# Optimization experiments

Measured on AMD Instinct MI355X. Metric: run time of the kernel, lower is better.

The kernel has to match this reference:

```python
import jax, jax.numpy as jnp
import numpy as np
from jax import lax

A = 9                 # 3 ratios x 3 scales
STRIDE = 16
PRE_NMS = 6000
POST_NMS = 300
NMS_THRESH = 0.7
POOL = 7
SAMPLES = 2           # roi-align sampling ratio
N_CLASSES = 21


def _generate_anchors(base=16.0, ratios=(0.5, 1.0, 2.0), scales=(8.0, 16.0, 32.0)):
    ratios = np.asarray(ratios, np.float64)
    scales = np.asarray(scales, np.float64)
    ctr = (base - 1.0) / 2.0
    size = base * base
    ws = np.round(np.sqrt(size / ratios))
    hs = np.round(ws * ratios)
    out = []
    for w0, h0 in zip(ws, hs):
        w2 = w0 * scales
        h2 = h0 * scales
        out.append(np.stack([ctr - (w2 - 1) / 2, ctr - (h2 - 1) / 2,
                             ctr + (w2 - 1) / 2, ctr + (h2 - 1) / 2], 1))
    return np.concatenate(out, 0).astype(np.float32)  # [A,4]


def _decode(anchors, deltas):
    # bbox_transform_inv with +1 width/height convention
    w = anchors[:, 2] - anchors[:, 0] + 1.0
    h = anchors[:, 3] - anchors[:, 1] + 1.0
    cx = anchors[:, 0] + 0.5 * w
    cy = anchors[:, 1] + 0.5 * h
    pcx = deltas[:, 0] * w + cx
    pcy = deltas[:, 1] * h + cy
    pw = jnp.exp(deltas[:, 2]) * w
    ph = jnp.exp(deltas[:, 3]) * h
    return jnp.stack([pcx - 0.5 * pw, pcy - 0.5 * ph,
                      pcx + 0.5 * pw, pcy + 0.5 * ph], 1)


def _nms_keep(boxes, thresh):
    # greedy NMS over score-sorted boxes; precomputed [N,N] IoU (memory-bound)
    N = boxes.shape[0]
    x1, y1, x2, y2 = boxes[:, 0], boxes[:, 1], boxes[:, 2], boxes[:, 3]
    areas = (x2 - x1 + 1.0) * (y2 - y1 + 1.0)
    xx1 = jnp.maximum(x1[:, None], x1[None, :])
    yy1 = jnp.maximum(y1[:, None], y1[None, :])
    xx2 = jnp.minimum(x2[:, None], x2[None, :])
    yy2 = jnp.minimum(y2[:, None], y2[None, :])
    inter = jnp.maximum(xx2 - xx1 + 1.0, 0.0) * jnp.maximum(yy2 - yy1 + 1.0, 0.0)
    iou = inter / (areas[:, None] + areas[None, :] - inter)
    ridx = jnp.arange(N)
    def body(i, supp):
        return supp | ((iou[i] > thresh) & (ridx > i) & ~supp[i])
    supp = lax.fori_loop(0, N, body, jnp.zeros((N,), bool))
    return ~supp


def _roi_align(feat, boxes, scale, out, ratio):
    # feat [C,H,W], boxes [R,4] in image coords -> [R,C,out,out]
    C, H, W = feat.shape
    R = boxes.shape[0]
    S = out * ratio
    x1 = boxes[:, 0] * scale
    y1 = boxes[:, 1] * scale
    x2 = boxes[:, 2] * scale
    y2 = boxes[:, 3] * scale
    bw = jnp.maximum(x2 - x1, 1.0) / out
    bh = jnp.maximum(y2 - y1, 1.0) / out
    off = (jnp.arange(S, dtype=feat.dtype) + 0.5) / ratio
    xs = jnp.clip(x1[:, None] + off[None, :] * bw[:, None], 0.0, W - 1.0)  # [R,S]
    ys = jnp.clip(y1[:, None] + off[None, :] * bh[:, None], 0.0, H - 1.0)
    x0 = jnp.floor(xs); y0 = jnp.floor(ys)
    lx = xs - x0; ly = ys - y0
    x0i = x0.astype(jnp.int32); x1i = jnp.minimum(x0i + 1, W - 1)
    y0i = y0.astype(jnp.int32); y1i = jnp.minimum(y0i + 1, H - 1)
    def g(yi, xi):  # gather -> [C,R,S,S]
        return feat[:, yi[:, :, None], xi[:, None, :]]
    wy0 = (1.0 - ly)[:, :, None]; wy1 = ly[:, :, None]
    wx0 = (1.0 - lx)[:, None, :]; wx1 = lx[:, None, :]
    val = (g(y0i, x0i) * (wy0 * wx0) + g(y0i, x1i) * (wy0 * wx1)
           + g(y1i, x0i) * (wy1 * wx0) + g(y1i, x1i) * (wy1 * wx1))
    pooled = val.reshape(C, R, out, ratio, out, ratio).mean(axis=(3, 5))
    return pooled.transpose(1, 0, 2, 3)


def setup_inputs() -> dict:
    key = jax.random.key(0)
    ks = jax.random.split(key, 8)
    base_feat = jax.random.normal(ks[0], (1, 1024, 64, 100), jnp.float32) * 0.5
    im_info = jnp.array([[1024.0, 1600.0, 1.0]], jnp.float32)  # H, W, scale
    rpn_conv_w = jax.random.normal(ks[1], (512, 1024, 3, 3), jnp.float32) * 0.01
    rpn_conv_b = jnp.zeros((512,), jnp.float32)
    rpn_cls_w = jax.random.normal(ks[2], (2 * A, 512), jnp.float32) * 0.01
    rpn_cls_b = jnp.zeros((2 * A,), jnp.float32)
    rpn_bbox_w = jax.random.normal(ks[3], (4 * A, 512), jnp.float32) * 0.01
    rpn_bbox_b = jnp.zeros((4 * A,), jnp.float32)
    fc_w = jax.random.normal(ks[4], (1024, 2048), jnp.float32) * 0.02
    fc_b = jnp.zeros((2048,), jnp.float32)
    cls_w = jax.random.normal(ks[5], (2048, N_CLASSES), jnp.float32) * 0.02
    cls_b = jnp.zeros((N_CLASSES,), jnp.float32)
    bbox_w = jax.random.normal(ks[6], (2048, 4 * N_CLASSES), jnp.float32) * 0.02
    bbox_b = jnp.zeros((4 * N_CLASSES,), jnp.float32)
    return dict(base_feat=base_feat, im_info=im_info,
                rpn_conv_w=rpn_conv_w, rpn_conv_b=rpn_conv_b,
                rpn_cls_w=rpn_cls_w, rpn_cls_b=rpn_cls_b,
                rpn_bbox_w=rpn_bbox_w, rpn_bbox_b=rpn_bbox_b,
                fc_w=fc_w, fc_b=fc_b, cls_w=cls_w, cls_b=cls_b,
                bbox_w=bbox_w, bbox_b=bbox_b)


def reference(base_feat, im_info, rpn_conv_w, rpn_conv_b, rpn_cls_w, rpn_cls_b,
              rpn_bbox_w, rpn_bbox_b, fc_w, fc_b, cls_w, cls_b, bbox_w, bbox_b):
    _, C, Hf, Wf = base_feat.shape
    # --- RPN head ---
    h = lax.conv_general_dilated(base_feat, rpn_conv_w, (1, 1), 'SAME',
                                 dimension_numbers=('NCHW', 'OIHW', 'NCHW'))
    h = jax.nn.relu(h + rpn_conv_b[None, :, None, None])
    cls_logits = jnp.einsum('nchw,oc->nohw', h, rpn_cls_w) + rpn_cls_b[None, :, None, None]
    bbox_out = jnp.einsum('nchw,oc->nohw', h, rpn_bbox_w) + rpn_bbox_b[None, :, None, None]
    # fg prob: channels are [bg(A), fg(A)] -> softmax over 2
    fg = jax.nn.softmax(cls_logits[0].reshape(2, A, Hf, Wf), axis=0)[1]  # [A,H,W]
    scores = fg.transpose(1, 2, 0).reshape(-1)                 # (H*W*A,)
    deltas = bbox_out[0].transpose(1, 2, 0).reshape(-1, 4)     # (H*W*A,4)
    # --- proposal layer ---
    anchors = jnp.asarray(_generate_anchors())
    sx = jnp.arange(Wf, dtype=jnp.float32) * STRIDE
    sy = jnp.arange(Hf, dtype=jnp.float32) * STRIDE
    gx, gy = jnp.meshgrid(sx, sy)                              # [H,W]
    shifts = jnp.stack([gx, gy, gx, gy], -1).reshape(-1, 4)    # [H*W,4]
    all_anchors = (shifts[:, None, :] + anchors[None, :, :]).reshape(-1, 4)
    boxes = _decode(all_anchors, deltas)
    im_h = im_info[0, 0]; im_w = im_info[0, 1]
    boxes = jnp.stack([jnp.clip(boxes[:, 0], 0.0, im_w - 1.0),
                       jnp.clip(boxes[:, 1], 0.0, im_h - 1.0),
                       jnp.clip(boxes[:, 2], 0.0, im_w - 1.0),
                       jnp.clip(boxes[:, 3], 0.0, im_h - 1.0)], 1)
    _, order = lax.top_k(scores, PRE_NMS)
    boxes_top = boxes[order]                                   # score-sorted desc
    keep = _nms_keep(boxes_top, NMS_THRESH)
    prio = keep.astype(jnp.float32) * (PRE_NMS - jnp.arange(PRE_NMS, dtype=jnp.float32))
    _, sel = lax.top_k(prio, POST_NMS)
    valid = keep[sel]
    roi_boxes = jnp.where(valid[:, None], boxes_top[sel], 0.0)  # zero-pad like original
    rois = jnp.concatenate([jnp.zeros((POST_NMS, 1), roi_boxes.dtype), roi_boxes], 1)
    # --- RoIAlign + head (proposals detached, as in the original) ---
    pooled = _roi_align(base_feat[0], lax.stop_gradient(roi_boxes), 1.0 / STRIDE, POOL, SAMPLES)
    vec = pooled.mean(axis=(2, 3))                             # [R,1024]
    hidden = jax.nn.relu(vec @ fc_w + fc_b)
    cls_prob = jax.nn.softmax(hidden @ cls_w + cls_b, axis=-1)
    bbox_pred = hidden @ bbox_w + bbox_b
    return rois, cls_prob, bbox_pred
```

## Files before the change

kernel.cpp:

```cpp
#include <hip/hip_runtime.h>


#define OFF_CLS   26214400u
#define OFF_BBOX  26675200u
#define OFF_BOXES 27596800u
#define OFF_KEYS  28518400u
#define OFF_HIST  28979200u
#define OFF_META  29241344u
#define OFF_RNK   29241600u
#define OFF_CAND  29472000u
#define OFF_BTOP  29702400u
#define OFF_MASK  29798400u
#define OFF_ROIB  34310400u
#define OFF_VEC   34315200u
#define OFF_HID   35544000u

__global__ __launch_bounds__(256) void k_conv(const float* __restrict__ in,
                                              const float* __restrict__ wgt,
                                              const float* __restrict__ bias,
                                              float* __restrict__ out) {
  const int tx = threadIdx.x;
  const int ty = threadIdx.y;
  const int pg = blockIdx.x * 64 + tx;
  const int p0 = pg * 4;
  const int y  = p0 / 100;
  const int x0 = p0 % 100;
  const int ocb = blockIdx.y * 32;
  const int tid = ty * 64 + tx;

  __shared__ float sw[32 * 9 * 36];

  float acc[8][4];
#pragma unroll
  for (int j = 0; j < 8; ++j)
#pragma unroll
    for (int q = 0; q < 4; ++q) acc[j][q] = 0.f;

  for (int icb = 0; icb < 1024; icb += 32) {
    __syncthreads();
    for (int k = tid; k < 32 * 288; k += 256) {
      int ocl = k / 288, r = k % 288;
      sw[r * 36 + ocl] = wgt[(size_t)(ocb + ocl) * 9216 + icb * 9 + r];
    }
    __syncthreads();

    for (int icl = 0; icl < 32; ++icl) {
      const float* pin = in + (size_t)(icb + icl) * 6400;
      float r[3][6];
#pragma unroll
      for (int dy = 0; dy < 3; ++dy) {
        int yy = y + dy - 1;
        bool vr = (yy >= 0) && (yy < 64);
        const float* prow = pin + yy * 100;
        float4 m = vr ? *(const float4*)(prow + x0) : make_float4(0.f, 0.f, 0.f, 0.f);
        r[dy][1] = m.x; r[dy][2] = m.y; r[dy][3] = m.z; r[dy][4] = m.w;
        r[dy][0] = (vr && x0 > 0)       ? prow[x0 - 1] : 0.f;
        r[dy][5] = (vr && x0 + 4 < 100) ? prow[x0 + 4] : 0.f;
      }
#pragma unroll
      for (int tap = 0; tap < 9; ++tap) {
        const int dy = tap / 3, kx = tap % 3;
        const float* swp = &sw[(icl * 9 + tap) * 36 + ty * 8];
        float4 w0 = *(const float4*)(swp);
        float4 w1 = *(const float4*)(swp + 4);
        float wv[8] = {w0.x, w0.y, w0.z, w0.w, w1.x, w1.y, w1.z, w1.w};
#pragma unroll
        for (int j = 0; j < 8; ++j)
#pragma unroll
          for (int q = 0; q < 4; ++q)
            acc[j][q] = fmaf(r[dy][q + kx], wv[j], acc[j][q]);
      }
    }
  }

#pragma unroll
  for (int j = 0; j < 8; ++j) {
    int oc = ocb + ty * 8 + j;
    float b = bias[oc];
#pragma unroll
    for (int q = 0; q < 4; ++q) {
      float v = acc[j][q] + b;
      out[(size_t)oc * 6400 + p0 + q] = fmaxf(v, 0.f);
    }
  }
}

__global__ __launch_bounds__(256) void k_rpn(const float* __restrict__ h,
                                             const float* __restrict__ cls_w,
                                             const float* __restrict__ cls_b,
                                             const float* __restrict__ bbox_w,
                                             const float* __restrict__ bbox_b,
                                             float* __restrict__ cls_out,
                                             float* __restrict__ bbox_out) {
  __shared__ float swt[64 * 56 + 16];
  const int tx = threadIdx.x, ty = threadIdx.y;
  const int tid = ty * 64 + tx;
  const int px = blockIdx.x * 64 + tx;

  float acc[16];
#pragma unroll
  for (int j = 0; j < 16; ++j) acc[j] = 0.f;

  for (int cb = 0; cb < 512; cb += 64) {
    __syncthreads();
    for (int k = tid; k < 64 * 54; k += 256) {
      int o = k / 64, cl = k % 64;
      swt[cl * 56 + o] = (o < 18) ? cls_w[o * 512 + cb + cl]
                                  : bbox_w[(o - 18) * 512 + cb + cl];
    }
    __syncthreads();
    for (int cl = 0; cl < 64; ++cl) {
      float hv = h[(size_t)(cb + cl) * 6400 + px];
      const float* wp = swt + cl * 56 + ty * 16;
      float4 w0 = *(const float4*)(wp);
      float4 w1 = *(const float4*)(wp + 4);
      float4 w2 = *(const float4*)(wp + 8);
      float4 w3 = *(const float4*)(wp + 12);
      acc[0]  = fmaf(hv, w0.x, acc[0]);  acc[1]  = fmaf(hv, w0.y, acc[1]);
      acc[2]  = fmaf(hv, w0.z, acc[2]);  acc[3]  = fmaf(hv, w0.w, acc[3]);
      acc[4]  = fmaf(hv, w1.x, acc[4]);  acc[5]  = fmaf(hv, w1.y, acc[5]);
      acc[6]  = fmaf(hv, w1.z, acc[6]);  acc[7]  = fmaf(hv, w1.w, acc[7]);
      acc[8]  = fmaf(hv, w2.x, acc[8]);  acc[9]  = fmaf(hv, w2.y, acc[9]);
      acc[10] = fmaf(hv, w2.z, acc[10]); acc[11] = fmaf(hv, w2.w, acc[11]);
      acc[12] = fmaf(hv, w3.x, acc[12]); acc[13] = fmaf(hv, w3.y, acc[13]);
      acc[14] = fmaf(hv, w3.z, acc[14]); acc[15] = fmaf(hv, w3.w, acc[15]);
    }
  }
#pragma unroll
  for (int j = 0; j < 16; ++j) {
    int o = ty * 16 + j;
    if (o < 54) {
      float v = acc[j] + ((o < 18) ? cls_b[o] : bbox_b[o - 18]);
      if (o < 18) cls_out[(size_t)o * 6400 + px] = v;
      else        bbox_out[(size_t)(o - 18) * 6400 + px] = v;
    }
  }
}

__global__ __launch_bounds__(256) void k_transpose(const float* __restrict__ in,
                                                   float* __restrict__ outp) {
  __shared__ float tile[64][65];
  const int tx = threadIdx.x, ty = threadIdx.y;
  const int cb = blockIdx.x * 64, pb = blockIdx.y * 64;
  for (int rr = ty; rr < 64; rr += 4)
    tile[rr][tx] = in[(size_t)(cb + rr) * 6400 + pb + tx];
  __syncthreads();
  for (int rr = ty; rr < 64; rr += 4)
    outp[(size_t)(pb + rr) * 1024 + cb + tx] = tile[tx][rr];
}

__global__ __launch_bounds__(256) void k_score(const float* __restrict__ cls,
                                               const float* __restrict__ bbx,
                                               const float* __restrict__ im_info,
                                               float4* __restrict__ boxes,
                                               unsigned long long* __restrict__ keys,
                                               unsigned int* __restrict__ hist) {
  const int i = blockIdx.x * 256 + threadIdx.x;
  if (i >= 57600) return;
  const int p = i / 9, a = i % 9;
  const int yy = p / 100, xx = p % 100;

  const float anc[9][4] = {
    {-84.f,-40.f,99.f,55.f},   {-176.f,-88.f,191.f,103.f}, {-360.f,-184.f,375.f,199.f},
    {-56.f,-56.f,71.f,71.f},   {-120.f,-120.f,135.f,135.f},{-248.f,-248.f,263.f,263.f},
    {-36.f,-80.f,51.f,95.f},   {-80.f,-168.f,95.f,183.f},  {-168.f,-344.f,183.f,359.f}};

  float l0 = cls[(size_t)a * 6400 + p];
  float l1 = cls[(size_t)(9 + a) * 6400 + p];
  float mx = fmaxf(l0, l1);
  float e0 = expf(l0 - mx), e1 = expf(l1 - mx);
  float sc = e1 / (e0 + e1);

  float d0 = bbx[(size_t)(4 * a + 0) * 6400 + p];
  float d1 = bbx[(size_t)(4 * a + 1) * 6400 + p];
  float d2 = bbx[(size_t)(4 * a + 2) * 6400 + p];
  float d3 = bbx[(size_t)(4 * a + 3) * 6400 + p];

  float ax1 = anc[a][0] + xx * 16.f, ay1 = anc[a][1] + yy * 16.f;
  float ax2 = anc[a][2] + xx * 16.f, ay2 = anc[a][3] + yy * 16.f;
  float w = ax2 - ax1 + 1.f, hh = ay2 - ay1 + 1.f;
  float cx = ax1 + 0.5f * w, cy = ay1 + 0.5f * hh;
  float pcx = d0 * w + cx, pcy = d1 * hh + cy;
  float pw = expf(d2) * w, ph = expf(d3) * hh;
  float bx1 = pcx - 0.5f * pw, by1 = pcy - 0.5f * ph;
  float bx2 = pcx + 0.5f * pw, by2 = pcy + 0.5f * ph;

  float imh = im_info[0], imw = im_info[1];
  bx1 = fminf(fmaxf(bx1, 0.f), imw - 1.f);
  by1 = fminf(fmaxf(by1, 0.f), imh - 1.f);
  bx2 = fminf(fmaxf(bx2, 0.f), imw - 1.f);
  by2 = fminf(fmaxf(by2, 0.f), imh - 1.f);

  boxes[i] = make_float4(bx1, by1, bx2, by2);
  unsigned sb = __float_as_uint(sc);
  keys[i] = ((unsigned long long)sb << 32) | (unsigned long long)(0xFFFFFFFFu - (unsigned)i);
  atomicAdd(&hist[sb >> 16], 1u);
}

__global__ __launch_bounds__(256) void k_cutoff(const unsigned int* __restrict__ hist,
                                                unsigned int* __restrict__ meta) {
  __shared__ unsigned csum[256];
  __shared__ unsigned sbin[256];
  __shared__ int schunk;
  __shared__ unsigned sacc;
  const int t = threadIdx.x;
  unsigned s = 0;
  for (int b = 0; b < 256; ++b) s += hist[t * 256 + b];
  csum[t] = s;
  __syncthreads();
  if (t == 0) {
    unsigned acc = 0; int tc = 0;
    for (int c = 255; c >= 0; --c) {
      if (acc + csum[c] >= 6000u) { tc = c; break; }
      acc += csum[c];
    }
    schunk = tc; sacc = acc;
  }
  __syncthreads();
  const int tc = schunk;
  sbin[t] = hist[tc * 256 + t];
  __syncthreads();
  if (t == 0) {
    unsigned acc = sacc; int bstar = tc * 256;
    for (int b = 255; b >= 0; --b) {
      acc += sbin[b];
      if (acc >= 6000u) { bstar = tc * 256 + b; break; }
    }
    meta[0] = (unsigned)bstar;
  }
}

__global__ __launch_bounds__(256) void k_compact(const unsigned long long* __restrict__ keys,
                                                 unsigned int* __restrict__ meta,
                                                 int* __restrict__ cand) {
  const int i = blockIdx.x * 256 + threadIdx.x;
  if (i >= 57600) return;
  unsigned bin = (unsigned)(keys[i] >> 48);
  if (bin >= meta[0]) {
    unsigned pos = atomicAdd(&meta[1], 1u);
    cand[pos] = i;
  }
}

__global__ __launch_bounds__(256) void k_rank(const unsigned long long* __restrict__ keys,
                                              const unsigned int* __restrict__ meta,
                                              const int* __restrict__ cand,
                                              int* __restrict__ rnk) {
  __shared__ unsigned long long sk[256];
  const int nc = (int)meta[1];
  if (blockIdx.x * 256 >= nc) return;
  const int cs = blockIdx.x * 256 + threadIdx.x;
  const bool act = cs < nc;
  const unsigned long long mk = act ? keys[cand[cs]] : ~0ull;
  int cnt = 0;
  const int base = blockIdx.y * 7200;
  for (int cb = 0; cb < 7200; cb += 256) {
    sk[threadIdx.x] = (cb + threadIdx.x < 7200) ? keys[base + cb + threadIdx.x] : 0ull;
    __syncthreads();
    if (act) {
#pragma unroll 8
      for (int j = 0; j < 256; ++j) cnt += (sk[j] > mk) ? 1 : 0;
    }
    __syncthreads();
  }
  if (act && cnt) atomicAdd(&rnk[cs], cnt);
}

__global__ __launch_bounds__(256) void k_scatter(const float4* __restrict__ boxes,
                                                 const unsigned int* __restrict__ meta,
                                                 const int* __restrict__ cand,
                                                 const int* __restrict__ rnk,
                                                 float4* __restrict__ btop) {
  const int cs = blockIdx.x * 256 + threadIdx.x;
  if (cs < (int)meta[1]) {
    int r = rnk[cs];
    if (r < 6000) btop[r] = boxes[cand[cs]];
  }
}

__global__ __launch_bounds__(256) void k_mask(const float4* __restrict__ btop,
                                              unsigned long long* __restrict__ mask) {
  const int lane = threadIdx.x;
  const int i = blockIdx.y * 4 + threadIdx.y;
  const int w = blockIdx.x;
  const int j = w * 64 + lane;
  float4 bi = btop[i];
  float4 bj = (j < 6000) ? btop[j] : make_float4(0.f, 0.f, 0.f, 0.f);
  float ai = (bi.z - bi.x + 1.f) * (bi.w - bi.y + 1.f);
  float aj = (bj.z - bj.x + 1.f) * (bj.w - bj.y + 1.f);
  float xx1 = fmaxf(bi.x, bj.x), yy1 = fmaxf(bi.y, bj.y);
  float xx2 = fminf(bi.z, bj.z), yy2 = fminf(bi.w, bj.w);
  float inter = fmaxf(xx2 - xx1 + 1.f, 0.f) * fmaxf(yy2 - yy1 + 1.f, 0.f);
  float iou = inter / (ai + aj - inter);
  bool sup = (j < 6000) && (j > i) && (iou > 0.7f);
  unsigned long long bal = __ballot(sup);
  if (lane == 0) mask[(size_t)i * 94 + w] = bal;
}

__global__ __launch_bounds__(64) void k_nms_scan(const unsigned long long* __restrict__ mask,
                                                 const float4* __restrict__ btop,
                                                 float4* __restrict__ roib,
                                                 float* __restrict__ rois) {
  const int lane = threadIdx.x;
  for (int k = lane; k < 1500; k += 64) rois[k] = 0.f;
  {
    float4 z = make_float4(0.f, 0.f, 0.f, 0.f);
    for (int k = lane; k < 300; k += 64) roib[k] = z;
  }
  unsigned long long sLo = 0ull, sHi = 0ull;
  unsigned long long pLo[8], pHi[8];
  float4 pBx[8];
#pragma unroll
  for (int u = 0; u < 8; ++u) {
    pLo[u] = mask[(size_t)u * 94 + lane];
    pHi[u] = (lane < 30) ? mask[(size_t)u * 94 + 64 + lane] : 0ull;
    pBx[u] = btop[u];
  }
  int kc = 0;
  for (int base = 0; base < 6000; base += 8) {
#pragma unroll
    for (int u = 0; u < 8; ++u) {
      const int i = base + u;
      unsigned long long rowLo = pLo[u], rowHi = pHi[u];
      float4 bx = pBx[u];
      const int ip = i + 8;
      if (ip < 6000) {
        pLo[u] = mask[(size_t)ip * 94 + lane];
        pHi[u] = (lane < 30) ? mask[(size_t)ip * 94 + 64 + lane] : 0ull;
        pBx[u] = btop[ip];
      }
      const int w = i >> 6, b = i & 63;
      unsigned long long cw = (w < 64) ? __shfl(sLo, w, 64) : __shfl(sHi, w - 64, 64);
      if (!((cw >> b) & 1ull)) {
        if (lane == 0) {
          rois[kc * 5 + 1] = bx.x; rois[kc * 5 + 2] = bx.y;
          rois[kc * 5 + 3] = bx.z; rois[kc * 5 + 4] = bx.w;
          roib[kc] = bx;
        }
        sLo |= rowLo;
        if (lane < 30) sHi |= rowHi;
        ++kc;
        if (kc >= 300) return;
      }
    }
  }
}

__global__ __launch_bounds__(256) void k_roialign(const float* __restrict__ ft,
                                                  const float4* __restrict__ roib,
                                                  float* __restrict__ vec) {
  const int r = blockIdx.x;
  const int tid = threadIdx.x;
  __shared__ int sx0[14], sx1[14], sy0[14], sy1[14];
  __shared__ float slx[14], sly[14];

  float4 bx = roib[r];
  float x1 = bx.x * 0.0625f, y1 = bx.y * 0.0625f;
  float x2 = bx.z * 0.0625f, y2 = bx.w * 0.0625f;
  float bw = fmaxf(x2 - x1, 1.0f) / 7.0f;
  float bh = fmaxf(y2 - y1, 1.0f) / 7.0f;
  if (tid < 14) {
    float off = ((float)tid + 0.5f) / 2.0f;
    float xs = fminf(fmaxf(x1 + off * bw, 0.f), 99.f);
    float x0f = floorf(xs);
    sx0[tid] = (int)x0f;
    sx1[tid] = min((int)x0f + 1, 99);
    slx[tid] = xs - x0f;
  } else if (tid < 28) {
    int t = tid - 14;
    float off = ((float)t + 0.5f) / 2.0f;
    float ys = fminf(fmaxf(y1 + off * bh, 0.f), 63.f);
    float y0f = floorf(ys);
    sy0[t] = (int)y0f;
    sy1[t] = min((int)y0f + 1, 63);
    sly[t] = ys - y0f;
  }
  __syncthreads();

  float ax = 0.f, ay = 0.f, az = 0.f, aw = 0.f;
  for (int py = 0; py < 7; ++py) {
    for (int px = 0; px < 7; ++px) {
      float cx_ = 0.f, cy_ = 0.f, cz_ = 0.f, cw_ = 0.f;
#pragma unroll
      for (int ss = 0; ss < 2; ++ss) {
        const int s = py * 2 + ss;
        const int yA = sy0[s], yB = sy1[s];
        const float ly = sly[s];
#pragma unroll
        for (int tt = 0; tt < 2; ++tt) {
          const int t = px * 2 + tt;
          const int xA = sx0[t], xB = sx1[t];
          const float lx = slx[t];
          const float w00 = (1.f - ly) * (1.f - lx), w01 = (1.f - ly) * lx;
          const float w10 = ly * (1.f - lx),         w11 = ly * lx;
          const float4 v00 = *(const float4*)(ft + ((size_t)(yA * 100 + xA) << 10) + (tid << 2));
          const float4 v01 = *(const float4*)(ft + ((size_t)(yA * 100 + xB) << 10) + (tid << 2));
          const float4 v10 = *(const float4*)(ft + ((size_t)(yB * 100 + xA) << 10) + (tid << 2));
          const float4 v11 = *(const float4*)(ft + ((size_t)(yB * 100 + xB) << 10) + (tid << 2));
          cx_ += v00.x * w00 + v01.x * w01 + v10.x * w10 + v11.x * w11;
          cy_ += v00.y * w00 + v01.y * w01 + v10.y * w10 + v11.y * w11;
          cz_ += v00.z * w00 + v01.z * w01 + v10.z * w10 + v11.z * w11;
          cw_ += v00.w * w00 + v01.w * w01 + v10.w * w10 + v11.w * w11;
        }
      }
      ax += cx_ * 0.25f; ay += cy_ * 0.25f; az += cz_ * 0.25f; aw += cw_ * 0.25f;
    }
  }
  float4 o;
  o.x = ax / 49.0f; o.y = ay / 49.0f; o.z = az / 49.0f; o.w = aw / 49.0f;
  *(float4*)(vec + (size_t)r * 1024 + (tid << 2)) = o;
}

__global__ __launch_bounds__(256) void k_fc1(const float* __restrict__ vec,
                                             const float* __restrict__ fw,
                                             const float* __restrict__ fb,
                                             float* __restrict__ hidden) {
  __shared__ float sa[12][1024];
  const int tx = threadIdx.x, ty = threadIdx.y;
  const int tid = ty * 64 + tx;
  const int nb = blockIdx.x * 256, mb = blockIdx.y * 12;

  for (int mm = 0; mm < 12; ++mm) {
    int m = mb + mm;
    float4 v = (m < 300) ? ((const float4*)(vec + (size_t)m * 1024))[tid]
                         : make_float4(0.f, 0.f, 0.f, 0.f);
    ((float4*)sa[mm])[tid] = v;
  }
  __syncthreads();

  const int n = nb + tx * 4;
  float acc[3][4];
#pragma unroll
  for (int mi = 0; mi < 3; ++mi)
#pragma unroll
    for (int q = 0; q < 4; ++q) acc[mi][q] = 0.f;

  for (int k = 0; k < 1024; ++k) {
    float4 b4 = *(const float4*)(fw + (size_t)k * 2048 + n);
#pragma unroll
    for (int mi = 0; mi < 3; ++mi) {
      float a = sa[ty * 3 + mi][k];
      acc[mi][0] = fmaf(a, b4.x, acc[mi][0]);
      acc[mi][1] = fmaf(a, b4.y, acc[mi][1]);
      acc[mi][2] = fmaf(a, b4.z, acc[mi][2]);
      acc[mi][3] = fmaf(a, b4.w, acc[mi][3]);
    }
  }
  float4 bias = *(const float4*)(fb + n);
#pragma unroll
  for (int mi = 0; mi < 3; ++mi) {
    int m = mb + ty * 3 + mi;
    if (m < 300) {
      float4 o;
      o.x = fmaxf(acc[mi][0] + bias.x, 0.f);
      o.y = fmaxf(acc[mi][1] + bias.y, 0.f);
      o.z = fmaxf(acc[mi][2] + bias.z, 0.f);
      o.w = fmaxf(acc[mi][3] + bias.w, 0.f);
      *(float4*)(hidden + (size_t)m * 2048 + n) = o;
    }
  }
}

__global__ __launch_bounds__(128) void k_head(const float* __restrict__ hidden,
                                              const float* __restrict__ cw,
                                              const float* __restrict__ cbias,
                                              const float* __restrict__ bw,
                                              const float* __restrict__ bbias,
                                              float* __restrict__ out_cls,
                                              float* __restrict__ out_bbox) {
  const int m = blockIdx.x, tid = threadIdx.x;
  __shared__ float sh[2048];
  __shared__ float slog[32];
  __shared__ float sred[2];
  for (int k = tid; k < 512; k += 128)
    ((float4*)sh)[k] = ((const float4*)(hidden + (size_t)m * 2048))[k];
  __syncthreads();
  if (tid < 21) {
    float a = 0.f;
#pragma unroll 4
    for (int k = 0; k < 2048; ++k) a = fmaf(sh[k], cw[(size_t)k * 21 + tid], a);
    slog[tid] = a + cbias[tid];
  } else if (tid < 105) {
    int j = tid - 21;
    float a = 0.f;
#pragma unroll 4
    for (int k = 0; k < 2048; ++k) a = fmaf(sh[k], bw[(size_t)k * 84 + j], a);
    out_bbox[(size_t)m * 84 + j] = a + bbias[j];
  }
  __syncthreads();
  if (tid == 0) {
    float mx = slog[0];
    for (int o = 1; o < 21; ++o) mx = fmaxf(mx, slog[o]);
    float sm = 0.f;
    for (int o = 0; o < 21; ++o) sm += expf(slog[o] - mx);
    sred[0] = mx; sred[1] = sm;
  }
  __syncthreads();
  if (tid < 21) out_cls[(size_t)m * 21 + tid] = expf(slog[tid] - sred[0]) / sred[1];
}

extern "C" void kernel_launch(void* const* d_in, const int* in_sizes, int n_in,
                              void* d_out, int out_size, void* d_ws, size_t ws_size,
                              hipStream_t stream) {
  const float* base_feat  = (const float*)d_in[0];
  const float* im_info    = (const float*)d_in[1];
  const float* rpn_conv_w = (const float*)d_in[2];
  const float* rpn_conv_b = (const float*)d_in[3];
  const float* rpn_cls_w  = (const float*)d_in[4];
  const float* rpn_cls_b  = (const float*)d_in[5];
  const float* rpn_bbox_w = (const float*)d_in[6];
  const float* rpn_bbox_b = (const float*)d_in[7];
  const float* fc_w   = (const float*)d_in[8];
  const float* fc_b   = (const float*)d_in[9];
  const float* cls_w  = (const float*)d_in[10];
  const float* cls_b  = (const float*)d_in[11];
  const float* bbox_w = (const float*)d_in[12];
  const float* bbox_b = (const float*)d_in[13];

  char* ws = (char*)d_ws;
  float* h     = (float*)(ws);
  float* ft    = (float*)(ws);
  float* clsL  = (float*)(ws + OFF_CLS);
  float* bboxL = (float*)(ws + OFF_BBOX);
  float4* boxes4 = (float4*)(ws + OFF_BOXES);
  unsigned long long* keys = (unsigned long long*)(ws + OFF_KEYS);
  unsigned int* hist = (unsigned int*)(ws + OFF_HIST);
  unsigned int* meta = (unsigned int*)(ws + OFF_META);
  int* rnk  = (int*)(ws + OFF_RNK);
  int* cand = (int*)(ws + OFF_CAND);
  float4* btop4 = (float4*)(ws + OFF_BTOP);
  unsigned long long* mask = (unsigned long long*)(ws + OFF_MASK);
  float4* roib4 = (float4*)(ws + OFF_ROIB);
  float* vec    = (float*)(ws + OFF_VEC);
  float* hidden = (float*)(ws + OFF_HID);

  float* out = (float*)d_out;

  hipMemsetAsync(ws + OFF_HIST, 0, 262144u + 256u + 230400u, stream);

  k_conv<<<dim3(25, 16), dim3(64, 4), 0, stream>>>(base_feat, rpn_conv_w, rpn_conv_b, h);
  k_rpn<<<dim3(100), dim3(64, 4), 0, stream>>>(h, rpn_cls_w, rpn_cls_b, rpn_bbox_w, rpn_bbox_b,
                                               clsL, bboxL);
  k_transpose<<<dim3(16, 100), dim3(64, 4), 0, stream>>>(base_feat, ft);
  k_score<<<dim3(225), dim3(256), 0, stream>>>(clsL, bboxL, im_info, boxes4, keys, hist);
  k_cutoff<<<dim3(1), dim3(256), 0, stream>>>(hist, meta);
  k_compact<<<dim3(225), dim3(256), 0, stream>>>(keys, meta, cand);
  k_rank<<<dim3(225, 8), dim3(256), 0, stream>>>(keys, meta, cand, rnk);
  k_scatter<<<dim3(225), dim3(256), 0, stream>>>(boxes4, meta, cand, rnk, btop4);
  k_mask<<<dim3(94, 1500), dim3(64, 4), 0, stream>>>(btop4, mask);
  k_nms_scan<<<dim3(1), dim3(64), 0, stream>>>(mask, btop4, roib4, out);
  k_roialign<<<dim3(300), dim3(256), 0, stream>>>(ft, roib4, vec);
  k_fc1<<<dim3(8, 25), dim3(64, 4), 0, stream>>>(vec, fc_w, fc_b, hidden);
  k_head<<<dim3(300), dim3(128), 0, stream>>>(hidden, cls_w, cls_b, bbox_w, bbox_b,
                                              out + 1500, out + 7800);
}
```

Measured before the change: 2.226 ms.

## Split RPN conv into single-wave blocks with register double-buffered input loads

The 3x3 RPN convolution now runs as 64-thread blocks that each own 8 output channels, giving a 25x64 grid instead of 25x16 blocks of 256 threads. The change targets poor occupancy on a 256-CU part, where only 400 blocks were available. Each block stages its weight slice into shared memory with float4 loads. Input rows for the next channel are prefetched into a second register buffer while the current one is consumed, and outputs are written as float4. The cost is that each input tile is now re-read by four times as many blocks, which adds global/L2 traffic, and the double buffer raises register pressure.

After: 2.307 ms. 1.04x slower.

```diff
diff --git a/kernel.cpp b/kernel.cpp
--- a/kernel.cpp
+++ b/kernel.cpp
@@ -15,74 +15,100 @@
 #define OFF_VEC   34315200u
 #define OFF_HID   35544000u
 
-__global__ __launch_bounds__(256) void k_conv(const float* __restrict__ in,
-                                              const float* __restrict__ wgt,
-                                              const float* __restrict__ bias,
-                                              float* __restrict__ out) {
-  const int tx = threadIdx.x;
-  const int ty = threadIdx.y;
-  const int pg = blockIdx.x * 64 + tx;
+__global__ __launch_bounds__(64) void k_conv(const float* __restrict__ in,
+                                             const float* __restrict__ wgt,
+                                             const float* __restrict__ bias,
+                                             float* __restrict__ out) {
+  const int lane = threadIdx.x;
+  const int pg = blockIdx.x * 64 + lane;
   const int p0 = pg * 4;
   const int y  = p0 / 100;
   const int x0 = p0 % 100;
-  const int ocb = blockIdx.y * 32;
-  const int tid = ty * 64 + tx;
-
-  __shared__ float sw[32 * 9 * 36];
+  const int ocb = blockIdx.y * 8;
+
+  __shared__ float sw[288 * 8];
 
   float acc[8][4];
 #pragma unroll
   for (int j = 0; j < 8; ++j)
 #pragma unroll
     for (int q = 0; q < 4; ++q) acc[j][q] = 0.f;
+
+  const bool vr_[3] = { (y - 1) >= 0, true, (y + 1) < 64 };
+  const bool le = (x0 > 0), re = (x0 + 4 < 100);
+
+  float bufA[3][6], bufB[3][6];
+
+#define LOADIC(R, IC)                                                          \
+  {                                                                            \
+    const float* pin = in + (size_t)(IC) * 6400;                               \
+    _Pragma("unroll")                                                          \
+    for (int dy = 0; dy < 3; ++dy) {                                           \
+      const int yy = y + dy - 1;                                               \
+      const bool vr = vr_[dy];                                                 \
+      const float* prow = pin + yy * 100;                                      \
+      float4 m = vr ? *(const float4*)(prow + x0)                              \
+                    : make_float4(0.f, 0.f, 0.f, 0.f);                         \
+      R[dy][1] = m.x; R[dy][2] = m.y; R[dy][3] = m.z; R[dy][4] = m.w;          \
+      R[dy][0] = (vr && le) ? prow[x0 - 1] : 0.f;                              \
+      R[dy][5] = (vr && re) ? prow[x0 + 4] : 0.f;                              \
+    }                                                                          \
+  }
+
+#define TAPS(R, ICL)                                                           \
+  {                                                                            \
+    _Pragma("unroll")                                                          \
+    for (int tap = 0; tap < 9; ++tap) {                                        \
+      const int dy = tap / 3, kx = tap % 3;                                    \
+      const float* swp = &sw[((ICL) * 9 + tap) * 8];                           \
+      float4 w0 = *(const float4*)(swp);                                       \
+      float4 w1 = *(const float4*)(swp + 4);                                   \
+      float wv[8] = {w0.x, w0.y, w0.z, w0.w, w1.x, w1.y, w1.z, w1.w};          \
+      _Pragma("unroll")                                                        \
+      for (int j = 0; j < 8; ++j)                                              \
+        _Pragma("unroll")                                                      \
+        for (int q = 0; q < 4; ++q)                                            \
+          acc[j][q] = fmaf(R[dy][q + kx], wv[j], acc[j][q]);                   \
+    }                                                                          \
+  }
+
+  LOADIC(bufA, 0);
 
   for (int icb = 0; icb < 1024; icb += 32) {
     __syncthreads();
-    for (int k = tid; k < 32 * 288; k += 256) {
-      int ocl = k / 288, r = k % 288;
-      sw[r * 36 + ocl] = wgt[(size_t)(ocb + ocl) * 9216 + icb * 9 + r];
+#pragma unroll
+    for (int k = lane; k < 576; k += 64) {
+      const int ocl = k / 72, r4 = k % 72;
+      float4 v = *(const float4*)(wgt + (size_t)(ocb + ocl) * 9216 + icb * 9 + r4 * 4);
+      sw[(r4 * 4 + 0) * 8 + ocl] = v.x;
+      sw[(r4 * 4 + 1) * 8 + ocl] = v.y;
+      sw[(r4 * 4 + 2) * 8 + ocl] = v.z;
+      sw[(r4 * 4 + 3) * 8 + ocl] = v.w;
     }
     __syncthreads();
 
-    for (int icl = 0; icl < 32; ++icl) {
-      const float* pin = in + (size_t)(icb + icl) * 6400;
-      float r[3][6];
-#pragma unroll
-      for (int dy = 0; dy < 3; ++dy) {
-        int yy = y + dy - 1;
-        bool vr = (yy >= 0) && (yy < 64);
-        const float* prow = pin + yy * 100;
-        float4 m = vr ? *(const float4*)(prow + x0) : make_float4(0.f, 0.f, 0.f, 0.f);
-        r[dy][1] = m.x; r[dy][2] = m.y; r[dy][3] = m.z; r[dy][4] = m.w;
-        r[dy][0] = (vr && x0 > 0)       ? prow[x0 - 1] : 0.f;
-        r[dy][5] = (vr && x0 + 4 < 100) ? prow[x0 + 4] : 0.f;
-      }
-#pragma unroll
-      for (int tap = 0; tap < 9; ++tap) {
-        const int dy = tap / 3, kx = tap % 3;
-        const float* swp = &sw[(icl * 9 + tap) * 36 + ty * 8];
-        float4 w0 = *(const float4*)(swp);
-        float4 w1 = *(const float4*)(swp + 4);
-        float wv[8] = {w0.x, w0.y, w0.z, w0.w, w1.x, w1.y, w1.z, w1.w};
-#pragma unroll
-        for (int j = 0; j < 8; ++j)
-#pragma unroll
-          for (int q = 0; q < 4; ++q)
-            acc[j][q] = fmaf(r[dy][q + kx], wv[j], acc[j][q]);
-      }
+    for (int icl = 0; icl < 32; icl += 2) {
+      const int ic = icb + icl;
+      LOADIC(bufB, ic + 1);
+      TAPS(bufA, icl);
+      if (ic + 2 < 1024) LOADIC(bufA, ic + 2);
+      TAPS(bufB, icl + 1);
     }
   }
 
 #pragma unroll
   for (int j = 0; j < 8; ++j) {
-    int oc = ocb + ty * 8 + j;
-    float b = bias[oc];
-#pragma unroll
-    for (int q = 0; q < 4; ++q) {
-      float v = acc[j][q] + b;
-      out[(size_t)oc * 6400 + p0 + q] = fmaxf(v, 0.f);
-    }
-  }
+    const int oc = ocb + j;
+    const float b = bias[oc];
+    float4 o;
+    o.x = fmaxf(acc[j][0] + b, 0.f);
+    o.y = fmaxf(acc[j][1] + b, 0.f);
+    o.z = fmaxf(acc[j][2] + b, 0.f);
+    o.w = fmaxf(acc[j][3] + b, 0.f);
+    *(float4*)(out + (size_t)oc * 6400 + p0) = o;
+  }
+#undef LOADIC
+#undef TAPS
 }
 
 __global__ __launch_bounds__(256) void k_rpn(const float* __restrict__ h,
@@ -538,7 +564,7 @@
 
   hipMemsetAsync(ws + OFF_HIST, 0, 262144u + 256u + 230400u, stream);
 
-  k_conv<<<dim3(25, 16), dim3(64, 4), 0, stream>>>(base_feat, rpn_conv_w, rpn_conv_b, h);
+  k_conv<<<dim3(25, 64), dim3(64), 0, stream>>>(base_feat, rpn_conv_w, rpn_conv_b, h);
   k_rpn<<<dim3(100), dim3(64, 4), 0, stream>>>(h, rpn_cls_w, rpn_cls_b, rpn_bbox_w, rpn_bbox_b,
                                                clsL, bboxL);
   k_transpose<<<dim3(16, 100), dim3(64, 4), 0, stream>>>(base_feat, ft);
```
